# Performance work log

Hardware: AMD Instinct MI355X
Metric: run time of the kernel (lower is better)

Reference implementation:

```python
import jax, jax.numpy as jnp
import numpy as np

B, C, H, W = 4, 512, 64, 64
D = 512  # model_dim


def setup_inputs() -> dict:
    key = jax.random.key(0)
    ks = jax.random.split(key, 9)
    s = 0.02
    return {
        "q": jax.random.normal(ks[0], (B, C, H, W), dtype=jnp.float32),
        "Wq": jax.random.normal(ks[1], (D, C), dtype=jnp.float32) * s,
        "bq": jax.random.normal(ks[2], (D,), dtype=jnp.float32) * s,
        "Wk": jax.random.normal(ks[3], (D, C), dtype=jnp.float32) * s,
        "bk": jax.random.normal(ks[4], (D,), dtype=jnp.float32) * s,
        "Wv": jax.random.normal(ks[5], (D, C), dtype=jnp.float32) * s,
        "bv": jax.random.normal(ks[6], (D,), dtype=jnp.float32) * s,
        "Wo": jax.random.normal(ks[7], (C, D), dtype=jnp.float32) * s,
        "bo": jax.random.normal(ks[8], (C,), dtype=jnp.float32) * s,
    }


def reference(q, Wq, bq, Wk, bk, Wv, bv, Wo, bo):
    b, c, h, w = q.shape
    # 1x1 conv == per-pixel linear over channels; tokens s = h*w
    x = q.reshape(b, c, h * w)                      # (b, c, s)
    Q = jnp.einsum('bcs,dc->bsd', x, Wq) + bq       # (b, s, D)
    K = jnp.einsum('bcs,dc->bsd', x, Wk) + bk
    V = jnp.einsum('bcs,dc->bsd', x, Wv) + bv
    # ScaleAttend: scale = q.shape[-1]^-0.5 = model_dim^-0.5 (heads not split)
    scale = jnp.asarray(Q.shape[-1], Q.dtype) ** -0.5
    sim = jnp.einsum('bsd,btd->bst', Q, K) * scale  # (b, s, s)
    attn = jax.nn.softmax(sim, axis=-1)
    o = jnp.einsum('bst,btd->bsd', attn, V)         # (b, s, D)
    # to_out 1x1 conv: D -> C
    y = jnp.einsum('bsd,cd->bsc', o, Wo) + bo       # (b, s, C)
    return y.transpose(0, 2, 1).reshape(b, c, h, w)
```

## Files before the change

### kernel.cpp

```cpp
#include <hip/hip_runtime.h>
#include <hip/hip_bf16.h>

typedef __hip_bfloat16 bf16;
typedef __attribute__((ext_vector_type(8))) short short8;
typedef __attribute__((ext_vector_type(4))) float floatx4;
typedef __attribute__((ext_vector_type(4))) short shortx4;

static constexpr int BATCH = 4;
static constexpr int CH    = 512;
static constexpr int SEQ   = 4096;
static constexpr int DM    = 512;

__device__ __forceinline__ void gload16(const void* g, void* l) {
  __builtin_amdgcn_global_load_lds(
      (const __attribute__((address_space(1))) unsigned int*)g,
      (__attribute__((address_space(3))) unsigned int*)l,
      16, 0, 0);
}

__global__ __launch_bounds__(256) void cvt_weights(
    const float* __restrict__ w0, const float* __restrict__ w1,
    const float* __restrict__ w2, const float* __restrict__ w3,
    bf16* __restrict__ out) {
  const float* src = (blockIdx.y == 0) ? w0 : (blockIdx.y == 1) ? w1
                   : (blockIdx.y == 2) ? w2 : w3;
  int idx = blockIdx.x * 256 + threadIdx.x;
  out[(long)blockIdx.y * (DM * CH) + idx] = __float2bfloat16(src[idx]);
}

__global__ __launch_bounds__(256) void transpose_cvt(
    const float* __restrict__ x, bf16* __restrict__ xT) {
  __shared__ float tile[64][65];
  const int s0 = blockIdx.x * 64, c0 = blockIdx.y * 64;
  const float* xb = x + (long)blockIdx.z * CH * SEQ;
  bf16* xTb = xT + (long)blockIdx.z * SEQ * CH;
  const int t = threadIdx.x;
  const int sl = t & 63, cq = t >> 6;
  #pragma unroll
  for (int i = 0; i < 16; ++i) {
    int cl = cq * 16 + i;
    tile[cl][sl] = xb[(long)(c0 + cl) * SEQ + s0 + sl];
  }
  __syncthreads();
  const int cl2 = t & 63, sq = t >> 6;
  #pragma unroll
  for (int i = 0; i < 16; ++i) {
    int sl2 = sq * 16 + i;
    xTb[(long)(s0 + sl2) * CH + c0 + cl2] = __float2bfloat16(tile[cl2][sl2]);
  }
}

template <int NREP, int MODE>
__global__ __launch_bounds__(512, 2) void gemm_big(
    const bf16* __restrict__ A, long sAz,
    const bf16* __restrict__ B, long sBz,
    void* __restrict__ Cv, long sCz,
    const float* __restrict__ bias, float scale,
    int K, int ldc) {
  constexpr int BN = NREP * 64;
  constexpr int BROUNDS = BN / 64;
  __shared__ __align__(16) bf16 As[2][256 * 64];
  __shared__ __align__(16) bf16 Bs[2][BN * 64];

  int id = blockIdx.x + gridDim.x * (blockIdx.y + gridDim.y * blockIdx.z);
  int nwg = gridDim.x * gridDim.y * gridDim.z;
  int sid = ((nwg & 7) == 0) ? ((id & 7) * (nwg >> 3) + (id >> 3)) : id;
  const int bx = sid % gridDim.x;
  const int by = (sid / gridDim.x) % gridDim.y;
  const int bz = sid / (gridDim.x * gridDim.y);

  const int tid = threadIdx.x;
  const long lK = K;
  const bf16* Ab = A + (long)bz * sAz + (long)by * 256 * lK;
  const bf16* Bb = B + (long)bz * sBz + (long)bx * BN * lK;

  const int w = tid >> 6, lane = tid & 63;
  const int wr = w >> 2, wc = w & 3;
  const int l16 = lane & 15, quad = lane >> 4;

  const int srow = tid >> 3;
  const int sp = tid & 7;
  const int slog = (sp ^ (srow & 7)) << 3;

  const int pA0 = (quad ^ (l16 & 7)) << 3;
  const int pA1 = pA0 ^ 32;

  auto stageA = [&](int buf, int kt) {
    const bf16* s = Ab + (long)kt * 64 + (long)srow * lK + slog;
    char* d = (char*)(&As[buf][0]) + tid * 16;
    #pragma unroll
    for (int r = 0; r < 4; ++r)
      gload16(s + (long)(r * 64) * lK, d + r * 8192);
  };
  auto stageB = [&](int buf, int kt) {
    const bf16* s = Bb + (long)kt * 64 + (long)srow * lK + slog;
    char* d = (char*)(&Bs[buf][0]) + tid * 16;
    #pragma unroll
    for (int r = 0; r < BROUNDS; ++r)
      gload16(s + (long)(r * 64) * lK, d + r * 8192);
  };

  floatx4 acc[8][NREP];
  #pragma unroll
  for (int m = 0; m < 8; ++m)
    #pragma unroll
    for (int n = 0; n < NREP; ++n) acc[m][n] = (floatx4)(0.0f);

  stageA(0, 0);
  stageB(0, 0);
  asm volatile("s_waitcnt vmcnt(0)" ::: "memory");
  __builtin_amdgcn_s_barrier();

  const int nk = K >> 6;
  int cur = 0;
  for (int t = 0; t < nk; ++t) {
    const bf16* __restrict__ Al = &As[cur][0];
    const bf16* __restrict__ Bl = &Bs[cur][0];
    const bool last = (t == nk - 1);
    short8 a[4];
    short8 b[2][NREP];
    #pragma unroll
    for (int p = 0; p < 4; ++p) {
      const int qm = p >> 1, kc = p & 1;
      const int poff = kc ? pA1 : pA0;
      #pragma unroll
      for (int i = 0; i < 4; ++i) {
        const int ar = wr * 128 + qm * 64 + i * 16 + l16;
        a[i] = *(const short8*)(Al + ar * 64 + poff);
      }
      if (qm == 0) {
        #pragma unroll
        for (int j = 0; j < NREP; ++j) {
          const int br = wc * (NREP * 16) + j * 16 + l16;
          b[kc][j] = *(const short8*)(Bl + br * 64 + poff);
        }
      }
      if (!last) {
        if (p == 0) stageA(cur ^ 1, t + 1);
        if (p == 1) stageB(cur ^ 1, t + 1);
      }
      __builtin_amdgcn_s_barrier();
      __builtin_amdgcn_s_setprio(1);
      #pragma unroll
      for (int i = 0; i < 4; ++i)
        #pragma unroll
        for (int j = 0; j < NREP; ++j)
          acc[qm * 4 + i][j] = __builtin_amdgcn_mfma_f32_16x16x32_bf16(
              a[i], b[kc][j], acc[qm * 4 + i][j], 0, 0, 0);
      __builtin_amdgcn_s_setprio(0);
      if (p == 3) {
        asm volatile("s_waitcnt vmcnt(0)" ::: "memory");
      }
      __builtin_amdgcn_s_barrier();
    }
    cur ^= 1;
  }

  const int rbase = by * 256 + wr * 128 + quad * 4;
  const int cbase = bx * BN + wc * (NREP * 16) + l16;
  #pragma unroll
  for (int m = 0; m < 8; ++m) {
    const int row = rbase + m * 16;
    #pragma unroll
    for (int n = 0; n < NREP; ++n) {
      const int col = cbase + n * 16;
      floatx4 v = acc[m][n];
      if constexpr (MODE == 0) {
        bf16* C = (bf16*)Cv + (long)bz * sCz;
        const float bb = bias[col];
        #pragma unroll
        for (int r = 0; r < 4; ++r)
          C[(long)(row + r) * ldc + col] = __float2bfloat16(v[r] + bb);
      } else if constexpr (MODE == 1) {
        bf16* C = (bf16*)Cv + (long)bz * sCz;
        const float bb = bias[col];
        alignas(8) bf16 tmp[4];
        #pragma unroll
        for (int r = 0; r < 4; ++r) tmp[r] = __float2bfloat16(v[r] + bb);
        *(shortx4*)(C + (long)col * ldc + row) = *(const shortx4*)tmp;
      } else if constexpr (MODE == 2) {
        bf16* C = (bf16*)Cv + (long)bz * sCz;
        #pragma unroll
        for (int r = 0; r < 4; ++r)
          C[(long)(row + r) * ldc + col] = __float2bfloat16(v[r] * scale);
      } else {
        float* C = (float*)Cv + (long)bz * sCz;
        const float bb = bias[col];
        floatx4 o_;
        #pragma unroll
        for (int r = 0; r < 4; ++r) o_[r] = v[r] + bb;
        *(floatx4*)(C + (long)col * ldc + row) = o_;
      }
    }
  }
}

__global__ __launch_bounds__(256) void softmax_rows(bf16* __restrict__ sim) {
  bf16* p = sim + (long)blockIdx.y * ((long)SEQ * SEQ) + (long)blockIdx.x * SEQ;
  uint4* p4 = (uint4*)p;
  const int t = threadIdx.x;
  union U { uint4 u; ushort h[8]; } d[2];
  d[0].u = p4[t];
  d[1].u = p4[t + 256];
  float v[16];
  float mx = -3.0e38f;
  #pragma unroll
  for (int i = 0; i < 16; ++i) {
    v[i] = __uint_as_float(((unsigned)d[i >> 3].h[i & 7]) << 16);
    mx = fmaxf(mx, v[i]);
  }
  #pragma unroll
  for (int o = 32; o > 0; o >>= 1) mx = fmaxf(mx, __shfl_xor(mx, o));
  __shared__ float redmax[4], redsum[4];
  if ((t & 63) == 0) redmax[t >> 6] = mx;
  __syncthreads();
  mx = fmaxf(fmaxf(redmax[0], redmax[1]), fmaxf(redmax[2], redmax[3]));
  float sum = 0.f;
  #pragma unroll
  for (int i = 0; i < 16; ++i) {
    v[i] = __expf(v[i] - mx);
    sum += v[i];
  }
  #pragma unroll
  for (int o = 32; o > 0; o >>= 1) sum += __shfl_xor(sum, o);
  if ((t & 63) == 0) redsum[t >> 6] = sum;
  __syncthreads();
  sum = redsum[0] + redsum[1] + redsum[2] + redsum[3];
  const float inv = 1.0f / sum;
  union Hb { __hip_bfloat16 h; ushort u; };
  #pragma unroll
  for (int i = 0; i < 16; ++i) {
    Hb hb;
    hb.h = __float2bfloat16(v[i] * inv);
    d[i >> 3].h[i & 7] = hb.u;
  }
  p4[t] = d[0].u;
  p4[t + 256] = d[1].u;
}

extern "C" void kernel_launch(void* const* d_in, const int* in_sizes, int n_in,
                              void* d_out, int out_size, void* d_ws,
                              size_t ws_size, hipStream_t stream) {
  const float* q  = (const float*)d_in[0];
  const float* Wq = (const float*)d_in[1];
  const float* bq = (const float*)d_in[2];
  const float* Wk = (const float*)d_in[3];
  const float* bk = (const float*)d_in[4];
  const float* Wv = (const float*)d_in[5];
  const float* bv = (const float*)d_in[6];
  const float* Wo = (const float*)d_in[7];
  const float* bo = (const float*)d_in[8];
  float* out = (float*)d_out;

  bf16* ws = (bf16*)d_ws;
  const long WSZ = (long)DM * CH;
  const long XSZ = (long)SEQ * CH;
  const long SSZ = (long)SEQ * SEQ;
  bf16* Wqb = ws;
  bf16* Wkb = Wqb + WSZ;
  bf16* Wvb = Wqb + 2 * WSZ;
  bf16* Wob = Wqb + 3 * WSZ;
  bf16* xT  = Wqb + 4 * WSZ;
  bf16* Qb  = xT + BATCH * XSZ;
  bf16* Kb  = Qb + BATCH * XSZ;
  bf16* Vt  = Kb + BATCH * XSZ;
  bf16* Ob  = Vt + BATCH * XSZ;
  bf16* Sim = Ob + BATCH * XSZ;

  cvt_weights<<<dim3(WSZ / 256, 4), 256, 0, stream>>>(Wq, Wk, Wv, Wo, ws);
  transpose_cvt<<<dim3(SEQ / 64, CH / 64, BATCH), 256, 0, stream>>>(q, xT);

  gemm_big<2, 0><<<dim3(4, 16, BATCH), 512, 0, stream>>>(
      xT, XSZ, Wqb, 0, Qb, XSZ, bq, 1.f, CH, DM);
  gemm_big<2, 0><<<dim3(4, 16, BATCH), 512, 0, stream>>>(
      xT, XSZ, Wkb, 0, Kb, XSZ, bk, 1.f, CH, DM);
  gemm_big<2, 1><<<dim3(4, 16, BATCH), 512, 0, stream>>>(
      xT, XSZ, Wvb, 0, Vt, XSZ, bv, 1.f, CH, SEQ);
  gemm_big<4, 2><<<dim3(16, 16, BATCH), 512, 0, stream>>>(
      Qb, XSZ, Kb, XSZ, Sim, SSZ, nullptr, 0.04419417382415922f, CH, SEQ);
  softmax_rows<<<dim3(SEQ, BATCH), 256, 0, stream>>>(Sim);
  gemm_big<2, 2><<<dim3(4, 16, BATCH), 512, 0, stream>>>(
      Sim, SSZ, Vt, XSZ, Ob, XSZ, nullptr, 1.0f, SEQ, DM);
  gemm_big<2, 4><<<dim3(4, 16, BATCH), 512, 0, stream>>>(
      Ob, XSZ, Wob, 0, out, XSZ, bo, 1.f, DM, SEQ);
}
```

Before: 382.1 us.

## Add triple-buffered 256x128 GEMM kernel with two blocks per CU

Adds a gemm_bn128 kernel with a 256x128 tile, 64-wide K steps, three-stage LDS buffering and launch bounds allowing two workgroups per CU. The projection, attention-times-V and output GEMMs now use it; the QK^T GEMM still uses gemm_big. The aim is more prefetch depth and higher occupancy, hiding global-load latency better. The diff's insertion point splits gemm_big's epilogue: the inserted MODE 2 block closes gemm_big early, and its original MODE 0/1/2/4 epilogue becomes gemm_bn128's. That is consistent, but it looks odd.

```diff
diff --git a/kernel.cpp b/kernel.cpp
--- a/kernel.cpp
+++ b/kernel.cpp
@@ -163,6 +163,123 @@
     const int row = rbase + m * 16;
     #pragma unroll
     for (int n = 0; n < NREP; ++n) {
+      const int col = cbase + n * 16;
+      floatx4 v = acc[m][n];
+      if constexpr (MODE == 2) {
+        bf16* C = (bf16*)Cv + (long)bz * sCz;
+        #pragma unroll
+        for (int r = 0; r < 4; ++r)
+          C[(long)(row + r) * ldc + col] = __float2bfloat16(v[r] * scale);
+      }
+    }
+  }
+}
+
+template <int MODE>
+__global__ __launch_bounds__(512, 2) void gemm_bn128(
+    const bf16* __restrict__ A, long sAz,
+    const bf16* __restrict__ B, long sBz,
+    void* __restrict__ Cv, long sCz,
+    const float* __restrict__ bias, float scale,
+    int K, int ldc) {
+  __shared__ __align__(16) bf16 As[3][256 * 64];
+  __shared__ __align__(16) bf16 Bs[3][128 * 64];
+
+  int id = blockIdx.x + gridDim.x * (blockIdx.y + gridDim.y * blockIdx.z);
+  int nwg = gridDim.x * gridDim.y * gridDim.z;
+  int sid = ((nwg & 7) == 0) ? ((id & 7) * (nwg >> 3) + (id >> 3)) : id;
+  const int bx = sid % gridDim.x;
+  const int by = (sid / gridDim.x) % gridDim.y;
+  const int bz = sid / (gridDim.x * gridDim.y);
+
+  const int tid = threadIdx.x;
+  const long lK = K;
+  const bf16* Ab = A + (long)bz * sAz + (long)by * 256 * lK;
+  const bf16* Bb = B + (long)bz * sBz + (long)bx * 128 * lK;
+
+  const int w = tid >> 6, lane = tid & 63;
+  const int wr = w >> 1, wc = w & 1;
+  const int l16 = lane & 15, quad = lane >> 4;
+
+  const int srow = tid >> 3;
+  const int sp = tid & 7;
+  const int slog = (sp ^ (srow & 7)) << 3;
+
+  const int pA0 = (quad ^ (l16 & 7)) << 3;
+  const int pA1 = pA0 ^ 32;
+
+  auto stageA = [&](int buf, int kt) {
+    const bf16* s = Ab + (long)kt * 64 + (long)srow * lK + slog;
+    char* d = (char*)(&As[buf][0]) + tid * 16;
+    #pragma unroll
+    for (int r = 0; r < 4; ++r)
+      gload16(s + (long)(r * 64) * lK, d + r * 8192);
+  };
+  auto stageB = [&](int buf, int kt) {
+    const bf16* s = Bb + (long)kt * 64 + (long)srow * lK + slog;
+    char* d = (char*)(&Bs[buf][0]) + tid * 16;
+    #pragma unroll
+    for (int r = 0; r < 2; ++r)
+      gload16(s + (long)(r * 64) * lK, d + r * 8192);
+  };
+
+  floatx4 acc[4][4];
+  #pragma unroll
+  for (int m = 0; m < 4; ++m)
+    #pragma unroll
+    for (int n = 0; n < 4; ++n) acc[m][n] = (floatx4)(0.0f);
+
+  const int nk = K >> 6;
+  stageA(0, 0); stageB(0, 0);
+  stageA(1, 1); stageB(1, 1);
+  asm volatile("s_waitcnt vmcnt(6)" ::: "memory");
+  __builtin_amdgcn_s_barrier();
+
+  int bcur = 0, bstage = 2;
+  for (int t = 0; t < nk; ++t) {
+    const bf16* __restrict__ Al = &As[bcur][0];
+    const bf16* __restrict__ Bl = &Bs[bcur][0];
+    const bool more = (t + 2 < nk);
+    #pragma unroll
+    for (int kc = 0; kc < 2; ++kc) {
+      const int poff = kc ? pA1 : pA0;
+      short8 a[4], b[4];
+      #pragma unroll
+      for (int i = 0; i < 4; ++i)
+        a[i] = *(const short8*)(Al + (wr * 64 + i * 16 + l16) * 64 + poff);
+      #pragma unroll
+      for (int j = 0; j < 4; ++j)
+        b[j] = *(const short8*)(Bl + (wc * 64 + j * 16 + l16) * 64 + poff);
+      if (more) {
+        if (kc == 0) stageA(bstage, t + 2);
+        else         stageB(bstage, t + 2);
+      }
+      __builtin_amdgcn_s_barrier();
+      __builtin_amdgcn_s_setprio(1);
+      #pragma unroll
+      for (int i = 0; i < 4; ++i)
+        #pragma unroll
+        for (int j = 0; j < 4; ++j)
+          acc[i][j] = __builtin_amdgcn_mfma_f32_16x16x32_bf16(
+              a[i], b[j], acc[i][j], 0, 0, 0);
+      __builtin_amdgcn_s_setprio(0);
+      if (kc == 1) {
+        if (more)            asm volatile("s_waitcnt vmcnt(6)" ::: "memory");
+        else if (t + 1 < nk) asm volatile("s_waitcnt vmcnt(0)" ::: "memory");
+      }
+      __builtin_amdgcn_s_barrier();
+    }
+    bcur = (bcur == 2) ? 0 : bcur + 1;
+    bstage = (bstage == 2) ? 0 : bstage + 1;
+  }
+
+  const int rbase = by * 256 + wr * 64 + quad * 4;
+  const int cbase = bx * 128 + wc * 64 + l16;
+  #pragma unroll
+  for (int m = 0; m < 4; ++m) {
+    const int row = rbase + m * 16;
+    #pragma unroll
+    for (int n = 0; n < 4; ++n) {
       const int col = cbase + n * 16;
       floatx4 v = acc[m][n];
       if constexpr (MODE == 0) {
@@ -270,17 +387,17 @@
   cvt_weights<<<dim3(WSZ / 256, 4), 256, 0, stream>>>(Wq, Wk, Wv, Wo, ws);
   transpose_cvt<<<dim3(SEQ / 64, CH / 64, BATCH), 256, 0, stream>>>(q, xT);
 
-  gemm_big<2, 0><<<dim3(4, 16, BATCH), 512, 0, stream>>>(
+  gemm_bn128<0><<<dim3(4, 16, BATCH), 512, 0, stream>>>(
       xT, XSZ, Wqb, 0, Qb, XSZ, bq, 1.f, CH, DM);
-  gemm_big<2, 0><<<dim3(4, 16, BATCH), 512, 0, stream>>>(
+  gemm_bn128<0><<<dim3(4, 16, BATCH), 512, 0, stream>>>(
       xT, XSZ, Wkb, 0, Kb, XSZ, bk, 1.f, CH, DM);
-  gemm_big<2, 1><<<dim3(4, 16, BATCH), 512, 0, stream>>>(
+  gemm_bn128<1><<<dim3(4, 16, BATCH), 512, 0, stream>>>(
       xT, XSZ, Wvb, 0, Vt, XSZ, bv, 1.f, CH, SEQ);
   gemm_big<4, 2><<<dim3(16, 16, BATCH), 512, 0, stream>>>(
       Qb, XSZ, Kb, XSZ, Sim, SSZ, nullptr, 0.04419417382415922f, CH, SEQ);
   softmax_rows<<<dim3(SEQ, BATCH), 256, 0, stream>>>(Sim);
-  gemm_big<2, 2><<<dim3(4, 16, BATCH), 512, 0, stream>>>(
+  gemm_bn128<2><<<dim3(4, 16, BATCH), 512, 0, stream>>>(
       Sim, SSZ, Vt, XSZ, Ob, XSZ, nullptr, 1.0f, SEQ, DM);
-  gemm_big<2, 4><<<dim3(4, 16, BATCH), 512, 0, stream>>>(
+  gemm_bn128<4><<<dim3(4, 16, BATCH), 512, 0, stream>>>(
       Ob, XSZ, Wob, 0, out, XSZ, bo, 1.f, DM, SEQ);
 }
```

Measured after the change: 357.1 us. -6.5%, faster.
